# Optimization experiments

Hardware: AMD Instinct MI355X
Metric: run time of the kernel (lower is better)

The kernel has to match this reference:

```python
import jax, jax.numpy as jnp
import numpy as np

H = 512          # hidden_size == input_size
K = 32768        # number of child cell inputs (lattice merge fan-in)


def setup_inputs() -> dict:
    key = jax.random.key(0)
    ks = jax.random.split(key, 8)
    s = 1.0 / np.sqrt(H)  # keep matmul outputs O(1)
    return {
        "input_": jax.random.normal(ks[0], (1, H), dtype=jnp.float32),
        "c_input": jax.random.normal(ks[1], (K, H), dtype=jnp.float32),
        "h_0": jax.random.normal(ks[2], (1, H), dtype=jnp.float32),
        "c_0": jax.random.normal(ks[3], (1, H), dtype=jnp.float32),
        "weight_ih": jax.random.normal(ks[4], (H, 3 * H), dtype=jnp.float32) * s,
        "weight_hh": jax.random.normal(ks[5], (H, 3 * H), dtype=jnp.float32) * s,
        "bias": jnp.zeros((3 * H,), dtype=jnp.float32),
        "alpha_weight_ih": jax.random.normal(ks[6], (H, H), dtype=jnp.float32) * s,
        "alpha_weight_hh": jax.random.normal(ks[7], (H, H), dtype=jnp.float32) * s,
    }


def reference(input_, c_input, h_0, c_0, weight_ih, weight_hh, bias,
              alpha_weight_ih, alpha_weight_hh):
    # Gate pre-activations: addmm(bias, h_0, W_hh) + input_ @ W_ih  -> [1, 3H]
    gates = h_0 @ weight_hh + bias + input_ @ weight_ih
    i, o, g = jnp.split(gates, 3, axis=1)        # each [1, H]
    i = jax.nn.sigmoid(i)
    o = jax.nn.sigmoid(o)
    g = jnp.tanh(g)

    # Variable-child softmax-weighted cell merge (non-empty c_input branch)
    alpha_wi = input_ @ alpha_weight_ih          # [1, H], broadcast over K
    alpha_wh = c_input @ alpha_weight_hh         # [K, H]
    alpha = jax.nn.sigmoid(alpha_wi + alpha_wh)  # [K, H]

    logits = jnp.concatenate([i, alpha], axis=0)  # [K+1, H]
    w = jnp.exp(logits)
    w = w / (w.sum(axis=0, keepdims=True) + 1e-12)

    merge = jnp.concatenate([g, c_input], axis=0)  # [K+1, H]
    c_1 = (merge * w).sum(axis=0, keepdims=True)   # [1, H]
    h_1 = o * jnp.tanh(c_1)                        # [1, H]
    return h_1, c_1
```

## Files before the change

kernel.cpp:

```cpp
#include <hip/hip_runtime.h>
#include <hip/hip_bf16.h>
#include <stdint.h>

#define Hdim 512
#define KC   32768

typedef __hip_bfloat16 bf16;
typedef __attribute__((ext_vector_type(8))) short short8;
typedef __attribute__((ext_vector_type(4))) float float4v;

__device__ __forceinline__ void gl_lds16(const bf16* g, bf16* l) {
  __builtin_amdgcn_global_load_lds(
      (const __attribute__((address_space(1))) unsigned int*)g,
      (__attribute__((address_space(3))) unsigned int*)l,
      16, 0, 0);
}

__device__ __forceinline__ unsigned int pack_bf16_trunc(float e0, float e1) {
  union { float f; unsigned int u; } a, b;
  a.f = e0; b.f = e1;
  return __builtin_amdgcn_perm(b.u, a.u, 0x07060302u);
}

__global__ void wt_kernel(const float* __restrict__ w, bf16* __restrict__ wt) {
  __shared__ float tile[64][65];
  const int t = threadIdx.x;
  const int tx = t & 63, tw = t >> 6;
  const int d0 = blockIdx.x * 64, h0 = blockIdx.y * 64;
#pragma unroll
  for (int r = 0; r < 16; ++r) {
    int row = r * 4 + tw;
    tile[row][tx] = w[(d0 + row) * Hdim + h0 + tx];
  }
  __syncthreads();
#pragma unroll
  for (int r = 0; r < 16; ++r) {
    int row = r * 4 + tw;
    wt[(size_t)(h0 + row) * Hdim + d0 + tx] = __float2bfloat16(tile[tx][row]);
  }
}

__global__ void prep_kernel(const float* __restrict__ input_, const float* __restrict__ h_0,
                            const float* __restrict__ w_ih, const float* __restrict__ w_hh,
                            const float* __restrict__ bias, const float* __restrict__ a_w_ih,
                            float* __restrict__ gates, float* __restrict__ awi) {
  __shared__ float inf_[Hdim], h0f[Hdim];
  __shared__ float red[4][64];
  const int t = threadIdx.x;
  const int lane = t & 63, wv = t >> 6;
  for (int i = t; i < Hdim; i += 256) { inf_[i] = input_[i]; h0f[i] = h_0[i]; }
  __syncthreads();
  const int j0 = blockIdx.x * 64;
  float acc = 0.f;
  if (j0 < 3 * Hdim) {
    const int j = j0 + lane;
    for (int d = wv * 128; d < wv * 128 + 128; ++d)
      acc += h0f[d] * w_hh[d * 3 * Hdim + j] + inf_[d] * w_ih[d * 3 * Hdim + j];
  } else {
    const int j = j0 - 3 * Hdim + lane;
    for (int d = wv * 128; d < wv * 128 + 128; ++d)
      acc += inf_[d] * a_w_ih[d * Hdim + j];
  }
  red[wv][lane] = acc;
  __syncthreads();
  if (t < 64) {
    float s = red[0][t] + red[1][t] + red[2][t] + red[3][t];
    if (j0 < 3 * Hdim) gates[j0 + t] = s + bias[j0 + t];
    else               awi[j0 - 3 * Hdim + t] = s;
  }
}

__global__ __launch_bounds__(256) void gemm_reduce_kernel(
    const float* __restrict__ c_input, const bf16* __restrict__ WT,
    const float* __restrict__ awi,
    float* __restrict__ pw, float* __restrict__ pwc) {
  __shared__ __align__(16) bf16 As[128 * 64];
  __shared__ __align__(16) bf16 Bs[128 * 64];
  __shared__ float red_w[2][128];
  __shared__ float red_wc[2][128];

  const int tid  = threadIdx.x;
  const int lane = tid & 63;
  const int wave = tid >> 6;
  const int wm   = wave & 1;
  const int wn   = wave >> 1;
  const int lm   = lane & 15;
  const int lq   = lane >> 4;

  const int kk0 = blockIdx.x * 128;
  const int h0  = blockIdx.y * 128;

  float4v acc[4][4];
#pragma unroll
  for (int i = 0; i < 4; ++i)
#pragma unroll
    for (int j = 0; j < 4; ++j)
      acc[i][j] = (float4v){0.f, 0.f, 0.f, 0.f};

  const int ldrow = wave * 8 + (lane >> 3);
  const int ldcol = (lane & 7) * 8;

  for (int d0 = 0; d0 < Hdim; d0 += 64) {
#pragma unroll
    for (int r = 0; r < 4; ++r)
      gl_lds16(WT + (size_t)(h0 + r * 32 + ldrow) * Hdim + d0 + ldcol,
               Bs + (r * 32 + wave * 8) * 64);
#pragma unroll
    for (int j = 0; j < 8; ++j) {
      const int f = j * 256 + tid;
      float4v v = *(const float4v*)(c_input + (size_t)(kk0 + (f >> 4)) * Hdim + d0 + (f & 15) * 4);
      unsigned long long p = (unsigned long long)pack_bf16_trunc(v[0], v[1])
                           | ((unsigned long long)pack_bf16_trunc(v[2], v[3]) << 32);
      *(unsigned long long*)(As + (size_t)f * 4) = p;
    }
    __builtin_amdgcn_s_waitcnt(0x0f70);
    __syncthreads();

#pragma unroll
    for (int ks = 0; ks < 2; ++ks) {
      short8 a[4], b[4];
#pragma unroll
      for (int mt = 0; mt < 4; ++mt)
        a[mt] = *(const short8*)(As + (wm * 64 + mt * 16 + lm) * 64 + ks * 32 + lq * 8);
#pragma unroll
      for (int nt = 0; nt < 4; ++nt)
        b[nt] = *(const short8*)(Bs + (wn * 64 + nt * 16 + lm) * 64 + ks * 32 + lq * 8);
#pragma unroll
      for (int mt = 0; mt < 4; ++mt)
#pragma unroll
        for (int nt = 0; nt < 4; ++nt)
          acc[mt][nt] = __builtin_amdgcn_mfma_f32_16x16x32_bf16(a[mt], b[nt], acc[mt][nt], 0, 0, 0);
    }
    __syncthreads();
  }

  float awi_l[4];
#pragma unroll
  for (int nt = 0; nt < 4; ++nt)
    awi_l[nt] = awi[h0 + wn * 64 + nt * 16 + lm];

  float sw[4] = {0.f, 0.f, 0.f, 0.f}, swc[4] = {0.f, 0.f, 0.f, 0.f};
#pragma unroll
  for (int nt = 0; nt < 4; ++nt) {
    const int h = h0 + wn * 64 + nt * 16 + lm;
#pragma unroll
    for (int mt = 0; mt < 4; ++mt) {
      const int kkb = kk0 + wm * 64 + mt * 16 + lq * 4;
#pragma unroll
      for (int r = 0; r < 4; ++r) {
        float v = acc[mt][nt][r] + awi_l[nt];
        float aval = 1.f / (1.f + __expf(-v));
        float e = __expf(aval);
        float c = c_input[(size_t)(kkb + r) * Hdim + h];
        sw[nt]  += e;
        swc[nt] += e * c;
      }
    }
  }
#pragma unroll
  for (int nt = 0; nt < 4; ++nt) {
    sw[nt]  += __shfl_xor(sw[nt], 16, 64);
    sw[nt]  += __shfl_xor(sw[nt], 32, 64);
    swc[nt] += __shfl_xor(swc[nt], 16, 64);
    swc[nt] += __shfl_xor(swc[nt], 32, 64);
  }
  if (lq == 0) {
#pragma unroll
    for (int nt = 0; nt < 4; ++nt) {
      red_w[wm][wn * 64 + nt * 16 + lm]  = sw[nt];
      red_wc[wm][wn * 64 + nt * 16 + lm] = swc[nt];
    }
  }
  __syncthreads();
  if (tid < 128) {
    pw[(size_t)blockIdx.x * Hdim + h0 + tid]  = red_w[0][tid] + red_w[1][tid];
    pwc[(size_t)blockIdx.x * Hdim + h0 + tid] = red_wc[0][tid] + red_wc[1][tid];
  }
}

__global__ void finalize_kernel(const float* __restrict__ pw, const float* __restrict__ pwc,
                                const float* __restrict__ gates, float* __restrict__ out) {
  int hh = blockIdx.x * 64 + threadIdx.x;
  float sw = 0.f, swc = 0.f;
  for (int kb = 0; kb < KC / 128; ++kb) {
    sw  += pw[(size_t)kb * Hdim + hh];
    swc += pwc[(size_t)kb * Hdim + hh];
  }
  float ipre = gates[hh], opre = gates[Hdim + hh], gpre = gates[2 * Hdim + hh];
  float ei = expf(1.f / (1.f + expf(-ipre)));
  float g  = tanhf(gpre);
  float o  = 1.f / (1.f + expf(-opre));
  float denom = ei + sw + 1e-12f;
  float c1 = (ei * g + swc) / denom;
  float h1 = o * tanhf(c1);
  out[hh]        = h1;
  out[Hdim + hh] = c1;
}

extern "C" void kernel_launch(void* const* d_in, const int* in_sizes, int n_in,
                              void* d_out, int out_size, void* d_ws, size_t ws_size,
                              hipStream_t stream) {
  const float* input_  = (const float*)d_in[0];
  const float* c_input = (const float*)d_in[1];
  const float* h_0     = (const float*)d_in[2];
  const float* w_ih    = (const float*)d_in[4];
  const float* w_hh    = (const float*)d_in[5];
  const float* bias    = (const float*)d_in[6];
  const float* a_w_ih  = (const float*)d_in[7];
  const float* a_w_hh  = (const float*)d_in[8];

  char* ws = (char*)d_ws;
  float* pw    = (float*)ws;
  float* pwc   = (float*)(ws + 512 * 1024);
  float* gates = (float*)(ws + 1024 * 1024);
  float* awi   = (float*)(ws + 1024 * 1024 + 8192);
  bf16*  WT    = (bf16*)(ws + 1024 * 1024 + 16384);

  hipLaunchKernelGGL(wt_kernel, dim3(8, 8), dim3(256), 0, stream, a_w_hh, WT);
  hipLaunchKernelGGL(prep_kernel, dim3(32), dim3(256), 0, stream,
                     input_, h_0, w_ih, w_hh, bias, a_w_ih, gates, awi);
  hipLaunchKernelGGL(gemm_reduce_kernel, dim3(KC / 128, Hdim / 128), dim3(256), 0, stream,
                     c_input, WT, awi, pw, pwc);
  hipLaunchKernelGGL(finalize_kernel, dim3(8), dim3(64), 0, stream,
                     pw, pwc, gates, (float*)d_out);
}
```

Measured before the change: 170.1 us.

## Merge prep kernels, swizzle LDS tiles, remap GEMM blocks, parallelize finalize

Fuses the weight-transpose and gate/awi projection kernels into one launch. The projection is split across 4 d-chunks with atomic accumulation into a memset buffer, and bias is moved to finalize. The GEMM now loads the B tile through registers instead of global_load_lds and writes both LDS tiles with an XOR swizzle to avoid bank conflicts. It also uses a 1D grid remapped so neighbouring blocks share the same K rows across H tiles, which should improve L2 reuse of c_input. Finalize uses 256 threads with a shared-memory reduction to shorten its serial loop, at the cost of an extra memset launch and atomics.

```diff
diff --git a/kernel.cpp b/kernel.cpp
--- a/kernel.cpp
+++ b/kernel.cpp
@@ -8,13 +8,6 @@
 typedef __hip_bfloat16 bf16;
 typedef __attribute__((ext_vector_type(8))) short short8;
 typedef __attribute__((ext_vector_type(4))) float float4v;
-
-__device__ __forceinline__ void gl_lds16(const bf16* g, bf16* l) {
-  __builtin_amdgcn_global_load_lds(
-      (const __attribute__((address_space(1))) unsigned int*)g,
-      (__attribute__((address_space(3))) unsigned int*)l,
-      16, 0, 0);
-}
 
 __device__ __forceinline__ unsigned int pack_bf16_trunc(float e0, float e1) {
   union { float f; unsigned int u; } a, b;
@@ -22,51 +15,63 @@
   return __builtin_amdgcn_perm(b.u, a.u, 0x07060302u);
 }
 
-__global__ void wt_kernel(const float* __restrict__ w, bf16* __restrict__ wt) {
-  __shared__ float tile[64][65];
+__global__ __launch_bounds__(256) void prep_wt_kernel(
+    const float* __restrict__ input_, const float* __restrict__ h_0,
+    const float* __restrict__ w_ih, const float* __restrict__ w_hh,
+    const float* __restrict__ a_w_ih, const float* __restrict__ a_w_hh,
+    float* __restrict__ gates, float* __restrict__ awi, bf16* __restrict__ wt) {
+  __shared__ float sh[64 * 65];
   const int t = threadIdx.x;
-  const int tx = t & 63, tw = t >> 6;
-  const int d0 = blockIdx.x * 64, h0 = blockIdx.y * 64;
-#pragma unroll
-  for (int r = 0; r < 16; ++r) {
-    int row = r * 4 + tw;
-    tile[row][tx] = w[(d0 + row) * Hdim + h0 + tx];
-  }
-  __syncthreads();
-#pragma unroll
-  for (int r = 0; r < 16; ++r) {
-    int row = r * 4 + tw;
-    wt[(size_t)(h0 + row) * Hdim + d0 + tx] = __float2bfloat16(tile[tx][row]);
-  }
-}
-
-__global__ void prep_kernel(const float* __restrict__ input_, const float* __restrict__ h_0,
-                            const float* __restrict__ w_ih, const float* __restrict__ w_hh,
-                            const float* __restrict__ bias, const float* __restrict__ a_w_ih,
-                            float* __restrict__ gates, float* __restrict__ awi) {
-  __shared__ float inf_[Hdim], h0f[Hdim];
-  __shared__ float red[4][64];
-  const int t = threadIdx.x;
-  const int lane = t & 63, wv = t >> 6;
-  for (int i = t; i < Hdim; i += 256) { inf_[i] = input_[i]; h0f[i] = h_0[i]; }
-  __syncthreads();
-  const int j0 = blockIdx.x * 64;
-  float acc = 0.f;
-  if (j0 < 3 * Hdim) {
-    const int j = j0 + lane;
-    for (int d = wv * 128; d < wv * 128 + 128; ++d)
-      acc += h0f[d] * w_hh[d * 3 * Hdim + j] + inf_[d] * w_ih[d * 3 * Hdim + j];
+  if (blockIdx.x < 128) {
+    const int b  = blockIdx.x;
+    const int jt = b & 31, dc = b >> 5;
+    const int lane = t & 63, wv = t >> 6;
+    float* h0s = sh;
+    float* ins = sh + 128;
+    float* red = sh + 256;
+    if (t < 128) { h0s[t] = h_0[dc * 128 + t]; ins[t] = input_[dc * 128 + t]; }
+    __syncthreads();
+    float acc = 0.f;
+    if (jt < 24) {
+      const int j = jt * 64 + lane;
+#pragma unroll 4
+      for (int i = 0; i < 32; ++i) {
+        const int dl = wv * 32 + i;
+        const size_t d = dc * 128 + dl;
+        acc += h0s[dl] * w_hh[d * 1536 + j] + ins[dl] * w_ih[d * 1536 + j];
+      }
+    } else {
+      const int j = (jt - 24) * 64 + lane;
+#pragma unroll 4
+      for (int i = 0; i < 32; ++i) {
+        const int dl = wv * 32 + i;
+        const size_t d = dc * 128 + dl;
+        acc += ins[dl] * a_w_ih[d * Hdim + j];
+      }
+    }
+    red[wv * 64 + lane] = acc;
+    __syncthreads();
+    if (t < 64) {
+      float s = red[t] + red[64 + t] + red[128 + t] + red[192 + t];
+      if (jt < 24) atomicAdd(&gates[jt * 64 + t], s);
+      else         atomicAdd(&awi[(jt - 24) * 64 + t], s);
+    }
   } else {
-    const int j = j0 - 3 * Hdim + lane;
-    for (int d = wv * 128; d < wv * 128 + 128; ++d)
-      acc += inf_[d] * a_w_ih[d * Hdim + j];
-  }
-  red[wv][lane] = acc;
-  __syncthreads();
-  if (t < 64) {
-    float s = red[0][t] + red[1][t] + red[2][t] + red[3][t];
-    if (j0 < 3 * Hdim) gates[j0 + t] = s + bias[j0 + t];
-    else               awi[j0 - 3 * Hdim + t] = s;
+    const int b = blockIdx.x - 128;
+    const int d0 = (b & 7) * 64, h0 = (b >> 3) * 64;
+    const int tx = t & 63, tw = t >> 6;
+    float (*tile)[65] = (float (*)[65])sh;
+#pragma unroll
+    for (int r = 0; r < 16; ++r) {
+      const int row = r * 4 + tw;
+      tile[row][tx] = a_w_hh[(size_t)(d0 + row) * Hdim + h0 + tx];
+    }
+    __syncthreads();
+#pragma unroll
+    for (int r = 0; r < 16; ++r) {
+      const int row = r * 4 + tw;
+      wt[(size_t)(h0 + row) * Hdim + d0 + tx] = __float2bfloat16(tile[tx][row]);
+    }
   }
 }
 
@@ -87,8 +92,11 @@
   const int lm   = lane & 15;
   const int lq   = lane >> 4;
 
-  const int kk0 = blockIdx.x * 128;
-  const int h0  = blockIdx.y * 128;
+  const int id     = blockIdx.x;
+  const int kk_idx = ((id >> 5) << 3) | (id & 7);
+  const int h_idx  = (id >> 3) & 3;
+  const int kk0 = kk_idx * 128;
+  const int h0  = h_idx * 128;
 
   float4v acc[4][4];
 #pragma unroll
@@ -97,34 +105,41 @@
     for (int j = 0; j < 4; ++j)
       acc[i][j] = (float4v){0.f, 0.f, 0.f, 0.f};
 
-  const int ldrow = wave * 8 + (lane >> 3);
-  const int ldcol = (lane & 7) * 8;
+  char* AsB = (char*)As;
+  char* BsB = (char*)Bs;
 
   for (int d0 = 0; d0 < Hdim; d0 += 64) {
-#pragma unroll
-    for (int r = 0; r < 4; ++r)
-      gl_lds16(WT + (size_t)(h0 + r * 32 + ldrow) * Hdim + d0 + ldcol,
-               Bs + (r * 32 + wave * 8) * 64);
 #pragma unroll
     for (int j = 0; j < 8; ++j) {
       const int f = j * 256 + tid;
-      float4v v = *(const float4v*)(c_input + (size_t)(kk0 + (f >> 4)) * Hdim + d0 + (f & 15) * 4);
+      const int row = f >> 4, sub = f & 15;
+      float4v v = *(const float4v*)(c_input + (size_t)(kk0 + row) * Hdim + d0 + sub * 4);
       unsigned long long p = (unsigned long long)pack_bf16_trunc(v[0], v[1])
                            | ((unsigned long long)pack_bf16_trunc(v[2], v[3]) << 32);
-      *(unsigned long long*)(As + (size_t)f * 4) = p;
-    }
-    __builtin_amdgcn_s_waitcnt(0x0f70);
+      *(unsigned long long*)(AsB + row * 128 + (((sub >> 1) ^ (row & 7)) * 16) + (sub & 1) * 8) = p;
+    }
+#pragma unroll
+    for (int r = 0; r < 4; ++r) {
+      const int row = r * 32 + wave * 8 + (lane >> 3);
+      const int g   = lane & 7;
+      short8 wv8 = *(const short8*)(WT + (size_t)(h0 + row) * Hdim + d0 + g * 8);
+      *(short8*)(BsB + row * 128 + ((g ^ (lane >> 3)) * 16)) = wv8;
+    }
     __syncthreads();
 
 #pragma unroll
     for (int ks = 0; ks < 2; ++ks) {
       short8 a[4], b[4];
 #pragma unroll
-      for (int mt = 0; mt < 4; ++mt)
-        a[mt] = *(const short8*)(As + (wm * 64 + mt * 16 + lm) * 64 + ks * 32 + lq * 8);
-#pragma unroll
-      for (int nt = 0; nt < 4; ++nt)
-        b[nt] = *(const short8*)(Bs + (wn * 64 + nt * 16 + lm) * 64 + ks * 32 + lq * 8);
+      for (int mt = 0; mt < 4; ++mt) {
+        const int row = wm * 64 + mt * 16 + lm;
+        a[mt] = *(const short8*)(AsB + row * 128 + (((ks * 4 + lq) ^ (lm & 7)) * 16));
+      }
+#pragma unroll
+      for (int nt = 0; nt < 4; ++nt) {
+        const int row = wn * 64 + nt * 16 + lm;
+        b[nt] = *(const short8*)(BsB + row * 128 + (((ks * 4 + lq) ^ (lm & 7)) * 16));
+      }
 #pragma unroll
       for (int mt = 0; mt < 4; ++mt)
 #pragma unroll
@@ -173,28 +188,43 @@
   }
   __syncthreads();
   if (tid < 128) {
-    pw[(size_t)blockIdx.x * Hdim + h0 + tid]  = red_w[0][tid] + red_w[1][tid];
-    pwc[(size_t)blockIdx.x * Hdim + h0 + tid] = red_wc[0][tid] + red_wc[1][tid];
-  }
-}
-
-__global__ void finalize_kernel(const float* __restrict__ pw, const float* __restrict__ pwc,
-                                const float* __restrict__ gates, float* __restrict__ out) {
-  int hh = blockIdx.x * 64 + threadIdx.x;
+    pw[(size_t)kk_idx * Hdim + h0 + tid]  = red_w[0][tid] + red_w[1][tid];
+    pwc[(size_t)kk_idx * Hdim + h0 + tid] = red_wc[0][tid] + red_wc[1][tid];
+  }
+}
+
+__global__ __launch_bounds__(256) void finalize_kernel(
+    const float* __restrict__ pw, const float* __restrict__ pwc,
+    const float* __restrict__ gates, const float* __restrict__ bias,
+    float* __restrict__ out) {
+  __shared__ float rsw[4][64], rswc[4][64];
+  const int t = threadIdx.x;
+  const int hl = t & 63, q = t >> 6;
+  const int hh = blockIdx.x * 64 + hl;
   float sw = 0.f, swc = 0.f;
-  for (int kb = 0; kb < KC / 128; ++kb) {
+#pragma unroll 4
+  for (int kb = q * 64; kb < q * 64 + 64; ++kb) {
     sw  += pw[(size_t)kb * Hdim + hh];
     swc += pwc[(size_t)kb * Hdim + hh];
   }
-  float ipre = gates[hh], opre = gates[Hdim + hh], gpre = gates[2 * Hdim + hh];
-  float ei = expf(1.f / (1.f + expf(-ipre)));
-  float g  = tanhf(gpre);
-  float o  = 1.f / (1.f + expf(-opre));
-  float denom = ei + sw + 1e-12f;
-  float c1 = (ei * g + swc) / denom;
-  float h1 = o * tanhf(c1);
-  out[hh]        = h1;
-  out[Hdim + hh] = c1;
+  rsw[q][hl] = sw; rswc[q][hl] = swc;
+  __syncthreads();
+  if (t < 64) {
+    const int h = blockIdx.x * 64 + t;
+    sw  = rsw[0][t] + rsw[1][t] + rsw[2][t] + rsw[3][t];
+    swc = rswc[0][t] + rswc[1][t] + rswc[2][t] + rswc[3][t];
+    float ipre = gates[h] + bias[h];
+    float opre = gates[Hdim + h] + bias[Hdim + h];
+    float gpre = gates[2 * Hdim + h] + bias[2 * Hdim + h];
+    float ei = expf(1.f / (1.f + expf(-ipre)));
+    float g  = tanhf(gpre);
+    float o  = 1.f / (1.f + expf(-opre));
+    float denom = ei + sw + 1e-12f;
+    float c1 = (ei * g + swc) / denom;
+    float h1 = o * tanhf(c1);
+    out[h]        = h1;
+    out[Hdim + h] = c1;
+  }
 }
 
 extern "C" void kernel_launch(void* const* d_in, const int* in_sizes, int n_in,
@@ -213,14 +243,14 @@
   float* pw    = (float*)ws;
   float* pwc   = (float*)(ws + 512 * 1024);
   float* gates = (float*)(ws + 1024 * 1024);
-  float* awi   = (float*)(ws + 1024 * 1024 + 8192);
-  bf16*  WT    = (bf16*)(ws + 1024 * 1024 + 16384);
-
-  hipLaunchKernelGGL(wt_kernel, dim3(8, 8), dim3(256), 0, stream, a_w_hh, WT);
-  hipLaunchKernelGGL(prep_kernel, dim3(32), dim3(256), 0, stream,
-                     input_, h_0, w_ih, w_hh, bias, a_w_ih, gates, awi);
-  hipLaunchKernelGGL(gemm_reduce_kernel, dim3(KC / 128, Hdim / 128), dim3(256), 0, stream,
+  float* awi   = (float*)(ws + 1024 * 1024 + 6144);
+  bf16*  WT    = (bf16*)(ws + 1024 * 1024 + 8192);
+
+  hipMemsetAsync(ws + 1024 * 1024, 0, 8192, stream);
+  hipLaunchKernelGGL(prep_wt_kernel, dim3(192), dim3(256), 0, stream,
+                     input_, h_0, w_ih, w_hh, a_w_ih, a_w_hh, gates, awi, WT);
+  hipLaunchKernelGGL(gemm_reduce_kernel, dim3(1024), dim3(256), 0, stream,
                      c_input, WT, awi, pw, pwc);
-  hipLaunchKernelGGL(finalize_kernel, dim3(8), dim3(64), 0, stream,
-                     pw, pwc, gates, (float*)d_out);
-}
+  hipLaunchKernelGGL(finalize_kernel, dim3(8), dim3(256), 0, stream,
+                     pw, pwc, gates, bias, (float*)d_out);
+}
```

Result: faster. 152.6 us (-10.3%).
